# Performance work log

Measured on AMD Instinct MI355X. Metric: run time of the kernel, lower is better.

Reference implementation:

```python
import jax, jax.numpy as jnp
import numpy as np

B, N, DIM = 2, 2048, 512
HEADS, DIM_HEAD = 8, 64
INNER = HEADS * DIM_HEAD  # 512
SCALE = DIM_HEAD ** -0.5


def setup_inputs() -> dict:
    key = jax.random.key(0)
    k1, k2, k3, k4, k5 = jax.random.split(key, 5)
    s = 0.02
    return {
        "x1": jax.random.normal(k1, (B, N, DIM), jnp.float32),
        "x2": jax.random.normal(k2, (B, N, DIM), jnp.float32),
        "W_qk": jax.random.normal(k3, (DIM, 2 * INNER), jnp.float32) * s,
        "W_v": jax.random.normal(k4, (DIM, INNER), jnp.float32) * s,
        "W_out": jax.random.normal(k5, (INNER, DIM), jnp.float32) * s,
        "b_out": jnp.zeros((DIM,), jnp.float32),
    }


def _split_heads(t):
    # [b, n, h*d] -> [b, h, n, d]
    b, n, _ = t.shape
    return t.reshape(b, n, HEADS, DIM_HEAD).transpose(0, 2, 1, 3)


def reference(x1, x2, W_qk, W_v, W_out, b_out):
    # to_qk(x1) -> chunk into k, v ; to_v(x2) -> q  (names in orig are swapped)
    kv = x1 @ W_qk                      # [b, n1, 2*inner]
    k, v = jnp.split(kv, 2, axis=-1)
    q = x2 @ W_v                        # [b, n2, inner]
    q, k, v = _split_heads(q), _split_heads(k), _split_heads(v)  # [b,h,n,d]
    dots = jnp.einsum("bhid,bhjd->bhij", q, k) * SCALE  # [b,h,n2,n1]
    attn = jax.nn.softmax(dots, axis=-1)
    out = jnp.einsum("bhij,bhjd->bhid", attn, v)         # [b,h,n2,d]
    out = out.transpose(0, 2, 1, 3).reshape(out.shape[0], out.shape[2], INNER)
    return out @ W_out + b_out          # [b, n2, dim]
```

## Files before the change

kernel.cpp:

```cpp
#include <hip/hip_runtime.h>

typedef short bf16x8 __attribute__((ext_vector_type(8)));
typedef short bf16x4 __attribute__((ext_vector_type(4)));
typedef float f32x4 __attribute__((ext_vector_type(4)));
typedef float f32x16 __attribute__((ext_vector_type(16)));
typedef unsigned short u16;
typedef unsigned int u32;
typedef u16 u16x8 __attribute__((ext_vector_type(8)));
typedef u16 u16x4 __attribute__((ext_vector_type(4)));

#define DEV __device__ __forceinline__

DEV u16 f2bf(float f) {
  unsigned u = __float_as_uint(f);
  u += 0x7fff + ((u >> 16) & 1);
  return (u16)(u >> 16);
}

DEV int pkbf(float lo, float hi) {
  return __builtin_amdgcn_perm(__float_as_uint(hi) + 0x8000u,
                               __float_as_uint(lo) + 0x8000u, 0x07060302u);
}

#define MFMA16(a, b, c) __builtin_amdgcn_mfma_f32_16x16x32_bf16(a, b, c, 0, 0, 0)
#define MFMA3216(a, b, c) __builtin_amdgcn_mfma_f32_32x32x16_bf16(a, b, c, 0, 0, 0)

#if __has_builtin(__builtin_amdgcn_mfma_f32_32x32x8bf16_1k)
#define HAVE_PV8 1
#define PVMFMA(a, b, c) __builtin_amdgcn_mfma_f32_32x32x8bf16_1k(a, b, c, 0, 0, 0)
#else
#define HAVE_PV8 0
#endif

#if __has_builtin(__builtin_amdgcn_exp2f)
#define QSCALE 0.18033688011112042f
#define EXPFN(x) __builtin_amdgcn_exp2f(x)
#else
#define QSCALE 0.125f
#define EXPFN(x) __expf(x)
#endif

#define GLD16(gp, lp)                                                     \
  __builtin_amdgcn_global_load_lds(                                       \
      (const __attribute__((address_space(1))) u32*)(gp),                 \
      (__attribute__((address_space(3))) u32*)(lp), 16, 0, 0)

__global__ __launch_bounds__(256) void wprep(
    const float* __restrict__ Wqk, const float* __restrict__ Wv,
    const float* __restrict__ Wout,
    u16* __restrict__ WqkT, u16* __restrict__ WvT, u16* __restrict__ WoutT) {
  __shared__ float tf[32][33];
  int bx = blockIdx.x, t = threadIdx.x;
  const float* src; u16* dst; int Ncols; int id;
  if (bx < 512)      { id = bx;       src = Wqk;  dst = WqkT;  Ncols = 1024; }
  else if (bx < 768) { id = bx - 512; src = Wv;   dst = WvT;   Ncols = 512; }
  else               { id = bx - 768; src = Wout; dst = WoutT; Ncols = 512; }
  int tilesPerRow = Ncols >> 5;
  int tr = id / tilesPerRow, tc = id % tilesPerRow;
  int r0 = tr * 32, c0 = tc * 32;
  {
    int r = t >> 3, c4 = (t & 7) * 4;
    float4 v = *(const float4*)(src + (long)(r0 + r) * Ncols + c0 + c4);
    tf[r][c4] = v.x; tf[r][c4 + 1] = v.y; tf[r][c4 + 2] = v.z; tf[r][c4 + 3] = v.w;
  }
  __syncthreads();
  {
    int c = t >> 3, r4 = (t & 7) * 4;
    u16x4 o;
    o[0] = f2bf(tf[r4][c]); o[1] = f2bf(tf[r4 + 1][c]);
    o[2] = f2bf(tf[r4 + 2][c]); o[3] = f2bf(tf[r4 + 3][c]);
    *(u16x4*)(dst + (long)(c0 + c) * 512 + r0 + r4) = o;
  }
}

__global__ __launch_bounds__(256) void qkv_gemm(
    const float* __restrict__ x1, const float* __restrict__ x2,
    const u16* __restrict__ WqkT, const u16* __restrict__ WvT,
    u16* __restrict__ out_q, u16* __restrict__ out_k, u16* __restrict__ out_vt) {
  __shared__ u16 sA[2][128 * 40];
  __shared__ u16 sB[2][64 * 40];
  int bx = blockIdx.x, t = threadIdx.x;
  bool isQ = bx < 256;
  int bx2 = isQ ? bx : bx - 256;
  const float* Ap = isQ ? x2 : x1;
  const u16* BT = isQ ? WvT : WqkT;
  int m0 = (bx2 & 31) * 128, n0 = (bx2 >> 5) * 64;
  int w = t >> 6, l = t & 63, lm = l & 15, lq = l >> 4;

  f32x4 zero = {0.f, 0.f, 0.f, 0.f};
  f32x4 acc[2][4];
#pragma unroll
  for (int i = 0; i < 2; ++i)
#pragma unroll
    for (int j = 0; j < 4; ++j) acc[i][j] = zero;

  int sm = t >> 2;
  int skc = (t & 3) * 8;
  const float* gAf = Ap + (long)(m0 + sm) * 512 + skc;
  const u16* gB = BT + (long)(n0 + sm) * 512 + skc;

  auto loadA = [&](int kt, int rows) {
    long off = (long)rows * 512 + kt * 32;
    float4 f0 = *(const float4*)(gAf + off);
    float4 f1 = *(const float4*)(gAf + off + 4);
    bf16x8 o;
    o[0] = (short)f2bf(f0.x); o[1] = (short)f2bf(f0.y);
    o[2] = (short)f2bf(f0.z); o[3] = (short)f2bf(f0.w);
    o[4] = (short)f2bf(f1.x); o[5] = (short)f2bf(f1.y);
    o[6] = (short)f2bf(f1.z); o[7] = (short)f2bf(f1.w);
    return o;
  };

  bf16x8 a0 = loadA(0, 0);
  bf16x8 a1 = loadA(0, 64);
  bf16x8 b0 = *(const bf16x8*)(gB);
  *(bf16x8*)(sA[0] + sm * 40 + skc) = a0;
  *(bf16x8*)(sA[0] + (sm + 64) * 40 + skc) = a1;
  *(bf16x8*)(sB[0] + sm * 40 + skc) = b0;
  __syncthreads();

  for (int kt = 0; kt < 16; ++kt) {
    int cur = kt & 1;
    if (kt < 15) {
      a0 = loadA(kt + 1, 0);
      a1 = loadA(kt + 1, 64);
      b0 = *(const bf16x8*)(gB + (kt + 1) * 32);
    }
    bf16x8 af[2], bfr[4];
    af[0] = *(const bf16x8*)(sA[cur] + (w * 32 + lm) * 40 + lq * 8);
    af[1] = *(const bf16x8*)(sA[cur] + (w * 32 + 16 + lm) * 40 + lq * 8);
#pragma unroll
    for (int s = 0; s < 4; ++s)
      bfr[s] = *(const bf16x8*)(sB[cur] + (s * 16 + lm) * 40 + lq * 8);
#pragma unroll
    for (int ms = 0; ms < 2; ++ms)
#pragma unroll
      for (int s = 0; s < 4; ++s)
        acc[ms][s] = MFMA16(af[ms], bfr[s], acc[ms][s]);
    if (kt < 15) {
      int nxt = 1 - cur;
      *(bf16x8*)(sA[nxt] + sm * 40 + skc) = a0;
      *(bf16x8*)(sA[nxt] + (sm + 64) * 40 + skc) = a1;
      *(bf16x8*)(sB[nxt] + sm * 40 + skc) = b0;
    }
    __syncthreads();
  }

#pragma unroll
  for (int ms = 0; ms < 2; ++ms) {
    int gmBase = m0 + w * 32 + ms * 16 + lq * 4;
#pragma unroll
    for (int s = 0; s < 4; ++s) {
      int gc = n0 + s * 16 + lm;
      int b = gmBase >> 11, n = gmBase & 2047;
      if (isQ) {
#pragma unroll
        for (int r = 0; r < 4; ++r)
          out_q[(((long)(b << 3) + (gc >> 6)) * 2048 + n + r) * 64 + (gc & 63)] =
              f2bf(acc[ms][s][r] * QSCALE);
      } else if (gc < 512) {
#pragma unroll
        for (int r = 0; r < 4; ++r)
          out_k[(((long)(b << 3) + (gc >> 6)) * 2048 + n + r) * 64 + (gc & 63)] =
              f2bf(acc[ms][s][r]);
      } else {
        int c = gc - 512, h = c >> 6, d = c & 63;
        u16x4 vv;
#pragma unroll
        for (int r = 0; r < 4; ++r) vv[r] = f2bf(acc[ms][s][r]);
        *(u16x4*)(out_vt + (((long)(b << 3) + h) * 64 + d) * 2048 + n) = vv;
      }
    }
  }
}

__global__ __launch_bounds__(256, 4) void attn(
    const u16* __restrict__ Q, const u16* __restrict__ K,
    const u16* __restrict__ Vt, u16* __restrict__ O) {
  int id = blockIdx.x;
  int bh = id & 15, qt = id >> 4;
  int b = bh >> 3, h = bh & 7;
  const u16* Kh = K + (long)bh * 2048 * 64;
  const u16* Vh = Vt + (long)bh * 64 * 2048;
  int t = threadIdx.x, w = t >> 6, lane = t & 63, ln = lane & 31, hi = lane >> 5;
  int g = w & 1, kh = w >> 1;

  __shared__ u16 smem[2][2][4096];
  u16* sKh = smem[0][kh];
  u16* sVh = smem[1][kh];

  bf16x8 qf[4];
  {
    const u16* qp = Q + (long)bh * 2048 * 64 + (long)(qt * 64 + g * 32 + ln) * 64 + hi * 8;
#pragma unroll
    for (int dc = 0; dc < 4; ++dc) qf[dc] = *(const bf16x8*)(qp + dc * 16);
  }

  f32x16 accO[2];
#pragma unroll
  for (int dt = 0; dt < 2; ++dt)
#pragma unroll
    for (int i = 0; i < 16; ++i) accO[dt][i] = 0.f;
  float dacc = 0.f;

  int lrow = lane >> 3;
  int swz = ((lane & 7) ^ lrow) * 8;
  const u16* gKl = Kh + (long)(kh * 1024 + g * 32 + lrow) * 64 + swz;
  const u16* gVl = Vh + (long)(g * 32 + lrow) * 2048 + kh * 1024 + swz;

  auto stage = [&](int jt) {
    const u16* gk = gKl + (long)jt * 4096;
    const u16* gv = gVl + jt * 64;
#pragma unroll
    for (int i = 0; i < 4; ++i) {
      GLD16(gk + i * 512, sKh + (g * 32 + i * 8) * 64);
      GLD16(gv + (long)i * 16384, sVh + (g * 32 + i * 8) * 64);
    }
  };

  stage(0);
  __syncthreads();

  int swl = ln & 7;
  for (int jt = 0; jt < 16; ++jt) {
#pragma unroll
    for (int kt2 = 0; kt2 < 2; ++kt2) {
      int rowK = (kt2 * 32 + ln) * 64;
      f32x16 st1, st2;
#pragma unroll
      for (int i = 0; i < 16; ++i) { st1[i] = 0.f; st2[i] = 0.f; }
      bf16x8 kf0 = *(const bf16x8*)(sKh + rowK + ((0 * 2 + hi) ^ swl) * 8);
      bf16x8 kf1 = *(const bf16x8*)(sKh + rowK + ((1 * 2 + hi) ^ swl) * 8);
      bf16x8 kf2 = *(const bf16x8*)(sKh + rowK + ((2 * 2 + hi) ^ swl) * 8);
      bf16x8 kf3 = *(const bf16x8*)(sKh + rowK + ((3 * 2 + hi) ^ swl) * 8);
      st1 = MFMA3216(kf0, qf[0], st1);
      st2 = MFMA3216(kf1, qf[1], st2);
      st1 = MFMA3216(kf2, qf[2], st1);
      st2 = MFMA3216(kf3, qf[3], st2);
      float p[16];
#pragma unroll
      for (int i = 0; i < 16; ++i) {
        float e = EXPFN(st1[i] + st2[i]);
        p[i] = e;
        dacc += e;
      }
#if HAVE_PV8
#pragma unroll
      for (int c = 0; c < 4; ++c) {
        union { int2 i2; bf16x4 v; } u;
        u.i2.x = pkbf(p[c * 4 + 0], p[c * 4 + 1]);
        u.i2.y = pkbf(p[c * 4 + 2], p[c * 4 + 3]);
#pragma unroll
        for (int dt = 0; dt < 2; ++dt) {
          bf16x4 vf = *(const bf16x4*)(sVh + (dt * 32 + ln) * 64 +
                                       (((kt2 * 4 + c) ^ swl) * 8) + hi * 4);
          accO[dt] = PVMFMA(vf, u.v, accO[dt]);
        }
      }
#else
#pragma unroll
      for (int c2 = 0; c2 < 2; ++c2) {
        int o0x = pkbf(p[c2 * 8 + 0], p[c2 * 8 + 1]);
        int o0y = pkbf(p[c2 * 8 + 2], p[c2 * 8 + 3]);
        int o1x = pkbf(p[c2 * 8 + 4], p[c2 * 8 + 5]);
        int o1y = pkbf(p[c2 * 8 + 6], p[c2 * 8 + 7]);
        int s0x = __shfl_xor(o0x, 32), s0y = __shfl_xor(o0y, 32);
        int s1x = __shfl_xor(o1x, 32), s1y = __shfl_xor(o1y, 32);
        union { int4 i4; bf16x8 v; } u;
        if (hi) { u.i4.x = s1x; u.i4.y = s1y; u.i4.z = o1x; u.i4.w = o1y; }
        else    { u.i4.x = o0x; u.i4.y = o0y; u.i4.z = s0x; u.i4.w = s0y; }
#pragma unroll
        for (int dt = 0; dt < 2; ++dt) {
          bf16x8 vf = *(const bf16x8*)(sVh + (dt * 32 + ln) * 64 +
                                       (((kt2 * 4 + c2 * 2 + hi) ^ swl) * 8));
          accO[dt] = MFMA3216(vf, u.v, accO[dt]);
        }
      }
#endif
    }
    __syncthreads();
    if (jt < 15) {
      stage(jt + 1);
      __syncthreads();
    }
  }

  float* cb = (float*)&smem[0][0][0];
  float* base = cb + g * 2112;
  if (kh == 1) {
#pragma unroll
    for (int dt = 0; dt < 2; ++dt)
#pragma unroll
      for (int i = 0; i < 16; ++i)
        base[(dt * 16 + i) * 64 + hi * 32 + ln] = accO[dt][i];
    base[2048 + hi * 32 + ln] = dacc;
  }
  __syncthreads();
  if (kh == 0) {
#pragma unroll
    for (int dt = 0; dt < 2; ++dt)
#pragma unroll
      for (int i = 0; i < 16; ++i)
        accO[dt][i] += base[(dt * 16 + i) * 64 + hi * 32 + ln];
    dacc += base[2048 + hi * 32 + ln];
    dacc += __shfl_xor(dacc, 32);
    float inv = 1.f / dacc;

    u16* Ob = O + ((long)b * 2048 + qt * 64 + g * 32 + ln) * 512 + h * 64;
#pragma unroll
    for (int dt = 0; dt < 2; ++dt)
#pragma unroll
      for (int gq = 0; gq < 4; ++gq) {
        u16x4 o;
#pragma unroll
        for (int rr = 0; rr < 4; ++rr) o[rr] = f2bf(accO[dt][gq * 4 + rr] * inv);
        *(u16x4*)(Ob + dt * 32 + gq * 8 + hi * 4) = o;
      }
  }
}

__global__ __launch_bounds__(128) void out_gemm(
    const u16* __restrict__ A, const u16* __restrict__ BT,
    float* __restrict__ out_f, const float* __restrict__ bias) {
  __shared__ u16 sA[2][64 * 40];
  __shared__ u16 sB[2][32 * 40];
  int t = threadIdx.x, bx = blockIdx.x;
  int m0 = (bx & 63) * 64, n0 = (bx >> 6) * 32;
  int w = t >> 6, l = t & 63, lm = l & 15, lq = l >> 4;

  f32x4 zero = {0.f, 0.f, 0.f, 0.f};
  f32x4 acc[2][2];
#pragma unroll
  for (int i = 0; i < 2; ++i)
#pragma unroll
    for (int j = 0; j < 2; ++j) acc[i][j] = zero;

  int ar = t >> 1, akc = (t & 1) * 16;
  int br = t >> 2, bkc = (t & 3) * 8;
  const u16* gA = A + (long)(m0 + ar) * 512 + akc;
  const u16* gB = BT + (long)(n0 + br) * 512 + bkc;

  bf16x8 a0 = *(const bf16x8*)(gA);
  bf16x8 a1 = *(const bf16x8*)(gA + 8);
  bf16x8 b0 = *(const bf16x8*)(gB);
  *(bf16x8*)(sA[0] + ar * 40 + akc) = a0;
  *(bf16x8*)(sA[0] + ar * 40 + akc + 8) = a1;
  *(bf16x8*)(sB[0] + br * 40 + bkc) = b0;
  __syncthreads();

  for (int kt = 0; kt < 16; ++kt) {
    int cur = kt & 1;
    if (kt < 15) {
      a0 = *(const bf16x8*)(gA + (kt + 1) * 32);
      a1 = *(const bf16x8*)(gA + (kt + 1) * 32 + 8);
      b0 = *(const bf16x8*)(gB + (kt + 1) * 32);
    }
    bf16x8 af[2], bfr[2];
    af[0] = *(const bf16x8*)(sA[cur] + (w * 32 + lm) * 40 + lq * 8);
    af[1] = *(const bf16x8*)(sA[cur] + (w * 32 + 16 + lm) * 40 + lq * 8);
    bfr[0] = *(const bf16x8*)(sB[cur] + (lm)*40 + lq * 8);
    bfr[1] = *(const bf16x8*)(sB[cur] + (16 + lm) * 40 + lq * 8);
#pragma unroll
    for (int ms = 0; ms < 2; ++ms)
#pragma unroll
      for (int s = 0; s < 2; ++s)
        acc[ms][s] = MFMA16(af[ms], bfr[s], acc[ms][s]);
    if (kt < 15) {
      int nxt = 1 - cur;
      *(bf16x8*)(sA[nxt] + ar * 40 + akc) = a0;
      *(bf16x8*)(sA[nxt] + ar * 40 + akc + 8) = a1;
      *(bf16x8*)(sB[nxt] + br * 40 + bkc) = b0;
    }
    __syncthreads();
  }

#pragma unroll
  for (int ms = 0; ms < 2; ++ms) {
    int gmBase = m0 + w * 32 + ms * 16 + lq * 4;
#pragma unroll
    for (int s = 0; s < 2; ++s) {
      int gc = n0 + s * 16 + lm;
      float bv = bias[gc];
#pragma unroll
      for (int r = 0; r < 4; ++r)
        out_f[(long)(gmBase + r) * 512 + gc] = acc[ms][s][r] + bv;
    }
  }
}

extern "C" void kernel_launch(void* const* d_in, const int* in_sizes, int n_in,
                              void* d_out, int out_size, void* d_ws, size_t ws_size,
                              hipStream_t stream) {
  const float* x1 = (const float*)d_in[0];
  const float* x2 = (const float*)d_in[1];
  const float* Wqk = (const float*)d_in[2];
  const float* Wv = (const float*)d_in[3];
  const float* Wout = (const float*)d_in[4];
  const float* bout = (const float*)d_in[5];
  float* out = (float*)d_out;

  u16* ws = (u16*)d_ws;
  const long SZ = 2097152;
  u16* Qw = ws;
  u16* Kw = ws + SZ;
  u16* Vtw = ws + 2 * SZ;
  u16* Ow = ws + 3 * SZ;
  u16* WqkT = ws + 4 * SZ;
  u16* WvT = WqkT + 524288;
  u16* WoutT = WvT + 262144;

  wprep<<<1024, 256, 0, stream>>>(Wqk, Wv, Wout, WqkT, WvT, WoutT);
  qkv_gemm<<<768, 256, 0, stream>>>(x1, x2, WqkT, WvT, Qw, Kw, Vtw);
  attn<<<512, 256, 0, stream>>>(Qw, Kw, Vtw, Ow);
  out_gemm<<<1024, 128, 0, stream>>>(Ow, WoutT, out, bout);
}
```

Measured before the change: 128.4 us.

## Split attention keys four ways per block with per-wave private LDS tiles

Each attention block now handles 32 queries instead of 64, and each of its four waves processes a private quarter of the keys using its own LDS K/V tiles, so the grid doubles to 1024 blocks. The block-wide __syncthreads inside the key loop are replaced by per-wave waitcnt barriers, which removes cross-wave stalls. Partial outputs and denominators from the four waves are combined through LDS at the end. In exchange, each block loads K/V once per 32 queries instead of once per 64, which doubles global and L2 traffic for K/V, and loads are no longer overlapped with compute.

Measured after the change: 130.0 us. No clear change (+1.3%).

```diff
diff --git a/kernel.cpp b/kernel.cpp
--- a/kernel.cpp
+++ b/kernel.cpp
@@ -44,6 +44,9 @@
   __builtin_amdgcn_global_load_lds(                                       \
       (const __attribute__((address_space(1))) u32*)(gp),                 \
       (__attribute__((address_space(3))) u32*)(lp), 16, 0, 0)
+
+#define WAIT_VM0 __builtin_amdgcn_s_waitcnt(0x0F70)
+#define WAIT_LGKM0 __builtin_amdgcn_s_waitcnt(0xC07F)
 
 __global__ __launch_bounds__(256) void wprep(
     const float* __restrict__ Wqk, const float* __restrict__ Wv,
@@ -183,15 +186,14 @@
   const u16* Kh = K + (long)bh * 2048 * 64;
   const u16* Vh = Vt + (long)bh * 64 * 2048;
   int t = threadIdx.x, w = t >> 6, lane = t & 63, ln = lane & 31, hi = lane >> 5;
-  int g = w & 1, kh = w >> 1;
-
-  __shared__ u16 smem[2][2][4096];
-  u16* sKh = smem[0][kh];
-  u16* sVh = smem[1][kh];
+
+  __shared__ u16 smem[4][2][2048];
+  u16* ktile = smem[w][0];
+  u16* vtile = smem[w][1];
 
   bf16x8 qf[4];
   {
-    const u16* qp = Q + (long)bh * 2048 * 64 + (long)(qt * 64 + g * 32 + ln) * 64 + hi * 8;
+    const u16* qp = Q + (long)bh * 2048 * 64 + (long)(qt * 32 + ln) * 64 + hi * 8;
 #pragma unroll
     for (int dc = 0; dc < 4; ++dc) qf[dc] = *(const bf16x8*)(qp + dc * 16);
   }
@@ -203,110 +205,114 @@
     for (int i = 0; i < 16; ++i) accO[dt][i] = 0.f;
   float dacc = 0.f;
 
-  int lrow = lane >> 3;
-  int swz = ((lane & 7) ^ lrow) * 8;
-  const u16* gKl = Kh + (long)(kh * 1024 + g * 32 + lrow) * 64 + swz;
-  const u16* gVl = Vh + (long)(g * 32 + lrow) * 2048 + kh * 1024 + swz;
+  int l8 = lane & 7, lr8 = lane >> 3;
+  int l4 = lane & 3, lr16 = lane >> 2;
+  const u16* gK0 = Kh + (long)(w * 512 + lr8) * 64 + (l8 ^ lr8) * 8;
+  const u16* gV0 = Vh + (long)lr16 * 2048 + w * 512 + (l4 ^ (lr16 & 3)) * 8;
 
   auto stage = [&](int jt) {
-    const u16* gk = gKl + (long)jt * 4096;
-    const u16* gv = gVl + jt * 64;
+    const u16* gk = gK0 + (long)jt * 2048;
+    const u16* gv = gV0 + jt * 32;
 #pragma unroll
     for (int i = 0; i < 4; ++i) {
-      GLD16(gk + i * 512, sKh + (g * 32 + i * 8) * 64);
-      GLD16(gv + (long)i * 16384, sVh + (g * 32 + i * 8) * 64);
+      GLD16(gk + i * 512, ktile + i * 512);
+      GLD16(gv + (long)i * 32768, vtile + i * 512);
     }
   };
 
   stage(0);
+  WAIT_VM0;
+
+  int s7 = ln & 7, s3 = ln & 3;
+  for (int jt = 0; jt < 16; ++jt) {
+    f32x16 st1, st2;
+#pragma unroll
+    for (int i = 0; i < 16; ++i) { st1[i] = 0.f; st2[i] = 0.f; }
+    bf16x8 kf0 = *(const bf16x8*)(ktile + ln * 64 + ((0 * 2 + hi) ^ s7) * 8);
+    bf16x8 kf1 = *(const bf16x8*)(ktile + ln * 64 + ((1 * 2 + hi) ^ s7) * 8);
+    bf16x8 kf2 = *(const bf16x8*)(ktile + ln * 64 + ((2 * 2 + hi) ^ s7) * 8);
+    bf16x8 kf3 = *(const bf16x8*)(ktile + ln * 64 + ((3 * 2 + hi) ^ s7) * 8);
+    st1 = MFMA3216(kf0, qf[0], st1);
+    st2 = MFMA3216(kf1, qf[1], st2);
+    st1 = MFMA3216(kf2, qf[2], st1);
+    st2 = MFMA3216(kf3, qf[3], st2);
+
+    float p[16];
+#pragma unroll
+    for (int i = 0; i < 16; ++i) {
+      float e = EXPFN(st1[i] + st2[i]);
+      p[i] = e;
+      dacc += e;
+    }
+
+#if HAVE_PV8
+#pragma unroll
+    for (int c = 0; c < 4; ++c) {
+      union { int2 i2; bf16x4 v; } u;
+      u.i2.x = pkbf(p[c * 4 + 0], p[c * 4 + 1]);
+      u.i2.y = pkbf(p[c * 4 + 2], p[c * 4 + 3]);
+#pragma unroll
+      for (int dt = 0; dt < 2; ++dt) {
+        bf16x4 vf = *(const bf16x4*)(vtile + (dt * 32 + ln) * 32 +
+                                     ((c ^ s3) * 8) + hi * 4);
+        accO[dt] = PVMFMA(vf, u.v, accO[dt]);
+      }
+    }
+#else
+#pragma unroll
+    for (int c2 = 0; c2 < 2; ++c2) {
+      int o0x = pkbf(p[c2 * 8 + 0], p[c2 * 8 + 1]);
+      int o0y = pkbf(p[c2 * 8 + 2], p[c2 * 8 + 3]);
+      int o1x = pkbf(p[c2 * 8 + 4], p[c2 * 8 + 5]);
+      int o1y = pkbf(p[c2 * 8 + 6], p[c2 * 8 + 7]);
+      int s0x = __shfl_xor(o0x, 32), s0y = __shfl_xor(o0y, 32);
+      int s1x = __shfl_xor(o1x, 32), s1y = __shfl_xor(o1y, 32);
+      union { int4 i4; bf16x8 v; } u;
+      if (hi) { u.i4.x = s1x; u.i4.y = s1y; u.i4.z = o1x; u.i4.w = o1y; }
+      else    { u.i4.x = o0x; u.i4.y = o0y; u.i4.z = s0x; u.i4.w = s0y; }
+#pragma unroll
+      for (int dt = 0; dt < 2; ++dt) {
+        bf16x8 vf = *(const bf16x8*)(vtile + (dt * 32 + ln) * 32 +
+                                     (((c2 * 2 + hi) ^ s3) * 8));
+        accO[dt] = MFMA3216(vf, u.v, accO[dt]);
+      }
+    }
+#endif
+
+    if (jt < 15) {
+      WAIT_LGKM0;
+      stage(jt + 1);
+      WAIT_VM0;
+    }
+  }
+
   __syncthreads();
-
-  int swl = ln & 7;
-  for (int jt = 0; jt < 16; ++jt) {
-#pragma unroll
-    for (int kt2 = 0; kt2 < 2; ++kt2) {
-      int rowK = (kt2 * 32 + ln) * 64;
-      f32x16 st1, st2;
-#pragma unroll
-      for (int i = 0; i < 16; ++i) { st1[i] = 0.f; st2[i] = 0.f; }
-      bf16x8 kf0 = *(const bf16x8*)(sKh + rowK + ((0 * 2 + hi) ^ swl) * 8);
-      bf16x8 kf1 = *(const bf16x8*)(sKh + rowK + ((1 * 2 + hi) ^ swl) * 8);
-      bf16x8 kf2 = *(const bf16x8*)(sKh + rowK + ((2 * 2 + hi) ^ swl) * 8);
-      bf16x8 kf3 = *(const bf16x8*)(sKh + rowK + ((3 * 2 + hi) ^ swl) * 8);
-      st1 = MFMA3216(kf0, qf[0], st1);
-      st2 = MFMA3216(kf1, qf[1], st2);
-      st1 = MFMA3216(kf2, qf[2], st1);
-      st2 = MFMA3216(kf3, qf[3], st2);
-      float p[16];
-#pragma unroll
-      for (int i = 0; i < 16; ++i) {
-        float e = EXPFN(st1[i] + st2[i]);
-        p[i] = e;
-        dacc += e;
-      }
-#if HAVE_PV8
-#pragma unroll
-      for (int c = 0; c < 4; ++c) {
-        union { int2 i2; bf16x4 v; } u;
-        u.i2.x = pkbf(p[c * 4 + 0], p[c * 4 + 1]);
-        u.i2.y = pkbf(p[c * 4 + 2], p[c * 4 + 3]);
-#pragma unroll
-        for (int dt = 0; dt < 2; ++dt) {
-          bf16x4 vf = *(const bf16x4*)(sVh + (dt * 32 + ln) * 64 +
-                                       (((kt2 * 4 + c) ^ swl) * 8) + hi * 4);
-          accO[dt] = PVMFMA(vf, u.v, accO[dt]);
-        }
-      }
-#else
-#pragma unroll
-      for (int c2 = 0; c2 < 2; ++c2) {
-        int o0x = pkbf(p[c2 * 8 + 0], p[c2 * 8 + 1]);
-        int o0y = pkbf(p[c2 * 8 + 2], p[c2 * 8 + 3]);
-        int o1x = pkbf(p[c2 * 8 + 4], p[c2 * 8 + 5]);
-        int o1y = pkbf(p[c2 * 8 + 6], p[c2 * 8 + 7]);
-        int s0x = __shfl_xor(o0x, 32), s0y = __shfl_xor(o0y, 32);
-        int s1x = __shfl_xor(o1x, 32), s1y = __shfl_xor(o1y, 32);
-        union { int4 i4; bf16x8 v; } u;
-        if (hi) { u.i4.x = s1x; u.i4.y = s1y; u.i4.z = o1x; u.i4.w = o1y; }
-        else    { u.i4.x = o0x; u.i4.y = o0y; u.i4.z = s0x; u.i4.w = s0y; }
-#pragma unroll
-        for (int dt = 0; dt < 2; ++dt) {
-          bf16x8 vf = *(const bf16x8*)(sVh + (dt * 32 + ln) * 64 +
-                                       (((kt2 * 4 + c2 * 2 + hi) ^ swl) * 8));
-          accO[dt] = MFMA3216(vf, u.v, accO[dt]);
-        }
-      }
-#endif
-    }
-    __syncthreads();
-    if (jt < 15) {
-      stage(jt + 1);
-      __syncthreads();
-    }
-  }
-
   float* cb = (float*)&smem[0][0][0];
-  float* base = cb + g * 2112;
-  if (kh == 1) {
+  if (w != 0) {
+    float* sc = cb + (w - 1) * 2112;
 #pragma unroll
     for (int dt = 0; dt < 2; ++dt)
 #pragma unroll
       for (int i = 0; i < 16; ++i)
-        base[(dt * 16 + i) * 64 + hi * 32 + ln] = accO[dt][i];
-    base[2048 + hi * 32 + ln] = dacc;
+        sc[(dt * 16 + i) * 64 + hi * 32 + ln] = accO[dt][i];
+    sc[2048 + hi * 32 + ln] = dacc;
   }
   __syncthreads();
-  if (kh == 0) {
-#pragma unroll
-    for (int dt = 0; dt < 2; ++dt)
-#pragma unroll
-      for (int i = 0; i < 16; ++i)
-        accO[dt][i] += base[(dt * 16 + i) * 64 + hi * 32 + ln];
-    dacc += base[2048 + hi * 32 + ln];
+  if (w == 0) {
+#pragma unroll
+    for (int j = 0; j < 3; ++j) {
+      float* sc = cb + j * 2112;
+#pragma unroll
+      for (int dt = 0; dt < 2; ++dt)
+#pragma unroll
+        for (int i = 0; i < 16; ++i)
+          accO[dt][i] += sc[(dt * 16 + i) * 64 + hi * 32 + ln];
+      dacc += sc[2048 + hi * 32 + ln];
+    }
     dacc += __shfl_xor(dacc, 32);
     float inv = 1.f / dacc;
 
-    u16* Ob = O + ((long)b * 2048 + qt * 64 + g * 32 + ln) * 512 + h * 64;
+    u16* Ob = O + ((long)b * 2048 + qt * 32 + ln) * 512 + h * 64;
 #pragma unroll
     for (int dt = 0; dt < 2; ++dt)
 #pragma unroll
@@ -411,6 +417,6 @@
 
   wprep<<<1024, 256, 0, stream>>>(Wqk, Wv, Wout, WqkT, WvT, WoutT);
   qkv_gemm<<<768, 256, 0, stream>>>(x1, x2, WqkT, WvT, Qw, Kw, Vtw);
-  attn<<<512, 256, 0, stream>>>(Qw, Kw, Vtw, Ow);
+  attn<<<1024, 256, 0, stream>>>(Qw, Kw, Vtw, Ow);
   out_gemm<<<1024, 128, 0, stream>>>(Ow, WoutT, out, bout);
 }
```
